# Kernel tuning notes

Hardware: AMD Instinct MI355X
Metric: run time of the kernel (lower is better)

## Reference

```python
import jax, jax.numpy as jnp
import numpy as np

ALPHA = 1.0
RANK = 4


def _conv2d_same(x, w):
    # x: [B,C,H,W], w: [O,C,kh,kw], stride 1, 'same' padding
    return jax.lax.conv_general_dilated(
        x, w, window_strides=(1, 1), padding='SAME',
        dimension_numbers=('NCHW', 'OIHW', 'NCHW'))


def setup_inputs() -> dict:
    key = jax.random.key(0)
    k1, k2, k3, k4, k5 = jax.random.split(key, 5)
    B, C, H, W = 32, 64, 64, 256
    O, E, r, k = 64, 4, RANK, 3
    x = jax.random.normal(k1, (B, C, H, W), dtype=jnp.float32)
    subject_id = jax.random.randint(k2, (B,), 0, E, dtype=jnp.int64)
    W_conv = jax.random.normal(k3, (O, C, k, k), dtype=jnp.float32) * (1.0 / np.sqrt(C * k * k))
    W_A = jax.random.normal(k4, (E, r, C, k, k), dtype=jnp.float32) * 0.02
    # torch init zeros W_B; use random here so the LoRA path is numerically exercised
    W_B = jax.random.normal(k5, (E, O, r), dtype=jnp.float32) * 0.02
    return {'x': x, 'subject_id': subject_id, 'W_conv': W_conv, 'W_A': W_A, 'W_B': W_B}


def reference(x, subject_id, W_conv, W_A, W_B):
    B, C, H, W = x.shape
    E, r = W_A.shape[0], W_A.shape[1]
    k = W_A.shape[-1]
    # Base conv
    out = _conv2d_same(x, W_conv)  # [B,O,H,W]
    # Run all adapter A-convs in one batched conv (E*r tiny output channels),
    # then per-sample select the adapter matching subject_id (same math as the
    # masked per-adapter dispatch in the original).
    a_all = _conv2d_same(x, W_A.reshape(E * r, C, k, k))  # [B,E*r,H,W]
    a_all = a_all.reshape(B, E, r, H, W)
    idx = subject_id[:, None, None, None, None]
    a_sel = jnp.take_along_axis(a_all, idx, axis=1)[:, 0]  # [B,r,H,W]
    wb_sel = W_B[subject_id]  # [B,O,r] (1x1 conv weight per sample)
    lora = (ALPHA / r) * jnp.einsum('bor,brhw->bohw', wb_sel, a_sel)
    return out + lora
```

## Files before the change

### kernel.cpp

```cpp
#include <hip/hip_runtime.h>
#include <hip/hip_bf16.h>

typedef __attribute__((ext_vector_type(8)))  short bf16x8;
typedef __attribute__((ext_vector_type(16))) float f32x16;

constexpr int Bn = 32, Cn = 64, Hn = 64, Wn = 256, On = 64, En = 4, Rn = 4;
constexpr float SCALE = 1.0f / Rn;

constexpr int WTILE  = 32;
constexpr int HSTRIP = 16;
constexpr int SLOT_B = 34 * 128;

__device__ __forceinline__ int swz(int ww, int cb) {
    return ww * 128 + ((cb ^ ((ww >> 2) & 7)) * 16);
}

__global__ __launch_bounds__(256) void merge_k(
    const float* __restrict__ Wc, const float* __restrict__ Wa,
    const float* __restrict__ Wb, __hip_bfloat16* __restrict__ Wfrag)
{
    int t = blockIdx.x * 256 + threadIdx.x;
    int j    = t & 7;
    int lane = (t >> 3) & 63;
    int g    = t >> 9;
    int s    = g % 36;
    int mh   = (g / 36) & 1;
    int e    = g / 72;
    int m = lane & 31, half = lane >> 5;
    int o = mh * 32 + m;
    int tap = s >> 2, cq = s & 3;
    int c = cq * 16 + half * 8 + j;
    float acc = Wc[(o * Cn + c) * 9 + tap];
#pragma unroll
    for (int r = 0; r < Rn; ++r)
        acc += SCALE * Wb[(e * On + o) * Rn + r] * Wa[((e * Rn + r) * Cn + c) * 9 + tap];
    Wfrag[t] = __float2bfloat16(acc);
}

__global__ __launch_bounds__(128, 2) void conv8_k(
    const float* __restrict__ x, const int* __restrict__ sid,
    const __hip_bfloat16* __restrict__ Wfrag, float* __restrict__ out)
{
    __shared__ __align__(16) char xs[4 * SLOT_B];

    const int tid = threadIdx.x;
    const int w0  = blockIdx.x * WTILE;
    const int h0  = blockIdx.y * HSTRIP;
    const int b   = blockIdx.z;
    const int e   = sid[b];
    const size_t HW = (size_t)Hn * Wn;

    const int lane = tid & 63, mh = tid >> 6;
    const int n = lane & 31, half = lane >> 5;

    bf16x8 wf[36];
    const bf16x8* wg = reinterpret_cast<const bf16x8*>(Wfrag) + (size_t)(e * 2 + mh) * 36 * 64;
#pragma unroll
    for (int s = 0; s < 36; ++s) wf[s] = wg[s * 64 + lane];

    const int pb = tid >> 3, q = tid & 7;
    const float* xbase = x + ((size_t)b * Cn + pb * 4) * HW + w0 + 4 * q;

    const int hside = tid >> 6, hc = tid & 63;
    const int gwh   = hside ? (w0 + WTILE) : (w0 - 1);
    const bool hv   = (unsigned)gwh < (unsigned)Wn;
    const float* hbase = x + ((size_t)b * Cn + hc) * HW + gwh;

    auto stage_load = [&](float4 (&f)[4], float& hx, int rx) {
        const int gh = h0 + rx;
        if ((unsigned)gh < (unsigned)Hn) {
            const float* src = xbase + (size_t)gh * Wn;
#pragma unroll
            for (int r = 0; r < 4; ++r)
                f[r] = *reinterpret_cast<const float4*>(src + r * HW);
            hx = hv ? hbase[(size_t)gh * Wn] : 0.0f;
        } else {
            float4 z4 = make_float4(0.0f, 0.0f, 0.0f, 0.0f);
#pragma unroll
            for (int r = 0; r < 4; ++r) f[r] = z4;
            hx = 0.0f;
        }
    };
    auto stage_store = [&](float4 (&f)[4], float& hx, int rx) {
        const int slot = (rx + 1) & 3;
        char* dbase = xs + slot * SLOT_B;
        const int cb = pb >> 1, sub = (pb & 1) * 8;
#pragma unroll
        for (int j = 0; j < 4; ++j) {
            union { __hip_bfloat16 u[4]; short4 v; } pk;
#pragma unroll
            for (int r = 0; r < 4; ++r) {
                float v = (j == 0) ? f[r].x : (j == 1) ? f[r].y : (j == 2) ? f[r].z : f[r].w;
                pk.u[r] = __float2bfloat16(v);
            }
            int ww = 4 * q + 1 + j;
            *reinterpret_cast<short4*>(dbase + swz(ww, cb) + sub) = pk.v;
        }
        {
            __hip_bfloat16 hb = __float2bfloat16(hx);
            int ww = hside ? (WTILE + 1) : 0;
            *reinterpret_cast<__hip_bfloat16*>(dbase + swz(ww, hc >> 3) + (hc & 7) * 2) = hb;
        }
    };

    auto barrier = [&]() {
        asm volatile("s_waitcnt lgkmcnt(0)" ::: "memory");
        __builtin_amdgcn_s_barrier();
    };

    float4 fA[4], fB[4];
    float  hxA, hxB;

    stage_load(fA, hxA, -1); stage_store(fA, hxA, -1);
    stage_load(fA, hxA, 0);  stage_store(fA, hxA, 0);
    stage_load(fA, hxA, 1);  stage_store(fA, hxA, 1);
    stage_load(fA, hxA, 2);
    barrier();

    for (int st = 0; st < HSTRIP; ++st) {
        const bool do_issue = (st + 3 <= HSTRIP);
        if (do_issue) {
            if (st & 1) stage_load(fA, hxA, st + 3);
            else        stage_load(fB, hxB, st + 3);
        }

        f32x16 a;
#pragma unroll
        for (int i = 0; i < 16; ++i) a[i] = 0.0f;

#pragma unroll
        for (int s = 0; s < 36; ++s) {
            const int tap = s >> 2, cq = s & 3;
            const int dh = tap / 3, dw = tap % 3;
            const int slotbase = ((st + dh) & 3) * SLOT_B;
            int ww = n + dw;
            bf16x8 bf = *reinterpret_cast<const bf16x8*>(xs + slotbase + swz(ww, cq * 2 + half));
            a = __builtin_amdgcn_mfma_f32_32x32x16_bf16(wf[s], bf, a, 0, 0, 0);
        }

        const bool do_store = (st + 2 <= HSTRIP);
        if (do_store) {
            if (st & 1) stage_store(fB, hxB, st + 2);
            else        stage_store(fA, hxA, st + 2);
        }

        {
            const int hrow = h0 + st;
            size_t base = ((size_t)(b * On + mh * 32 + 4 * half) * Hn + hrow) * Wn + w0 + n;
#pragma unroll
            for (int r = 0; r < 16; ++r) {
                int o_off = (r & 3) + 8 * (r >> 2);
                out[base + (size_t)o_off * HW] = a[r];
            }
        }

        barrier();
    }
}

extern "C" void kernel_launch(void* const* d_in, const int* in_sizes, int n_in,
                              void* d_out, int out_size, void* d_ws, size_t ws_size,
                              hipStream_t stream)
{
    const float* x   = (const float*)d_in[0];
    const int*   sid = (const int*)d_in[1];
    const float* Wc  = (const float*)d_in[2];
    const float* Wa  = (const float*)d_in[3];
    const float* Wb  = (const float*)d_in[4];
    float*       out = (float*)d_out;

    __hip_bfloat16* Wfrag = (__hip_bfloat16*)d_ws;

    merge_k<<<En * 2 * 36 * 64 * 8 / 256, 256, 0, stream>>>(Wc, Wa, Wb, Wfrag);

    dim3 grid(Wn / WTILE, Hn / HSTRIP, Bn);
    conv8_k<<<grid, 128, 0, stream>>>(x, sid, Wfrag, out);
}
```

Baseline: 273.5 us.

## Pre-pack input to swizzled bf16 NHWC and stream via global_load_lds

Adds a pack kernel that converts x to bf16 in a channel-last, swizzled, zero-padded row layout in workspace. The main conv kernel then copies rows straight into LDS with global_load_lds instead of per-thread fp32 loads, conversion and LDS stores. It also widens the tile to 64 columns with 4 waves and splits the MFMA chain across two accumulators. The cost is an extra full pass over x (fp32 read plus bf16 write) and a dependence on workspace size, with the old kernel kept as a fallback.

```diff
diff --git a/kernel.cpp b/kernel.cpp
--- a/kernel.cpp
+++ b/kernel.cpp
@@ -7,13 +7,20 @@
 constexpr int Bn = 32, Cn = 64, Hn = 64, Wn = 256, On = 64, En = 4, Rn = 4;
 constexpr float SCALE = 1.0f / Rn;
 
-constexpr int WTILE  = 32;
-constexpr int HSTRIP = 16;
-constexpr int SLOT_B = 34 * 128;
-
-__device__ __forceinline__ int swz(int ww, int cb) {
-    return ww * 128 + ((cb ^ ((ww >> 2) & 7)) * 16);
-}
+constexpr int ROW_B  = 258 * 128;
+
+constexpr int WTILE  = 64;
+constexpr int HSTRIP = 8;
+constexpr int SLOT_B = 66 * 128;
+
+constexpr size_t WFRAG_B = 294912;
+constexpr size_t XP_B    = (size_t)Bn * Hn * ROW_B;
+constexpr size_t ZROW_B  = ROW_B;
+
+#define GLOAD_LDS16(SRC, DST) \
+    __builtin_amdgcn_global_load_lds( \
+        (const __attribute__((address_space(1))) void*)(SRC), \
+        (__attribute__((address_space(3))) void*)(DST), 16, 0, 0)
 
 __global__ __launch_bounds__(256) void merge_k(
     const float* __restrict__ Wc, const float* __restrict__ Wa,
@@ -37,9 +44,48 @@
     Wfrag[t] = __float2bfloat16(acc);
 }
 
-__global__ __launch_bounds__(128, 2) void conv8_k(
-    const float* __restrict__ x, const int* __restrict__ sid,
-    const __hip_bfloat16* __restrict__ Wfrag, float* __restrict__ out)
+__global__ __launch_bounds__(256) void pack_k(
+    const float* __restrict__ x, __hip_bfloat16* __restrict__ xp,
+    __hip_bfloat16* __restrict__ zr)
+{
+    size_t g = (size_t)blockIdx.x * 256 + threadIdx.x;
+    if (blockIdx.x < 8192) {
+        int l  = (int)(g & 1023);
+        int cb = l & 7;
+        int p  = l >> 3;
+        int bh = (int)(g >> 10);
+        const float* xr = x + ((size_t)(bh >> 6) * Cn * Hn + (bh & 63)) * Wn;
+        union { __hip_bfloat16 u[8]; bf16x8 v; } u0, u1;
+#pragma unroll
+        for (int i = 0; i < 8; ++i) {
+            int c = cb * 8 + i;
+            float2 L = *reinterpret_cast<const float2*>(xr + (size_t)c * Hn * Wn + 2 * p);
+            u0.u[i] = __float2bfloat16(L.x);
+            u1.u[i] = __float2bfloat16(L.y);
+        }
+        char* row = (char*)xp + (size_t)bh * ROW_B;
+        int s0 = 2 * p + 1, s1 = 2 * p + 2;
+        *reinterpret_cast<bf16x8*>(row + s0 * 128 + ((cb ^ (s0 & 7)) * 16)) = u0.v;
+        *reinterpret_cast<bf16x8*>(row + s1 * 128 + ((cb ^ (s1 & 7)) * 16)) = u1.v;
+    } else if (blockIdx.x < 8192 + 128) {
+        int z = (int)(g - (size_t)8192 * 256);
+        int cb = z & 7, t = (z >> 3) & 1, bh = z >> 4;
+        char* row = (char*)xp + (size_t)bh * ROW_B;
+        bf16x8 zz = {};
+        *reinterpret_cast<bf16x8*>(row + (t ? 257 : 0) * 128 + cb * 16) = zz;
+    } else {
+        int t = (int)(g - (size_t)(8192 + 128) * 256);
+        if (t < ROW_B / 16) {
+            bf16x8 zz = {};
+            reinterpret_cast<bf16x8*>(zr)[t] = zz;
+        }
+    }
+}
+
+__global__ __launch_bounds__(256, 2) void conv9_k(
+    const __hip_bfloat16* __restrict__ xp, const __hip_bfloat16* __restrict__ zr,
+    const int* __restrict__ sid, const __hip_bfloat16* __restrict__ Wfrag,
+    float* __restrict__ out)
 {
     __shared__ __align__(16) char xs[4 * SLOT_B];
 
@@ -50,6 +96,98 @@
     const int e   = sid[b];
     const size_t HW = (size_t)Hn * Wn;
 
+    const int lane = tid & 63, wave = tid >> 6;
+    const int mh = wave & 1, nh = wave >> 1;
+    const int n = lane & 31, half = lane >> 5;
+
+    bf16x8 wf[36];
+    const bf16x8* wg = reinterpret_cast<const bf16x8*>(Wfrag) + (size_t)(e * 2 + mh) * 36 * 64;
+#pragma unroll
+    for (int s = 0; s < 36; ++s) wf[s] = wg[s * 64 + lane];
+
+    const char* xpb = (const char*)xp + (size_t)b * Hn * ROW_B + (size_t)w0 * 128;
+    const char* zrw = (const char*)zr + (size_t)w0 * 128;
+    const int lofs = wave * 1024 + lane * 16;
+
+    auto stage = [&](int rx) {
+        const int gh = h0 + rx;
+        const char* src = ((unsigned)gh < (unsigned)Hn) ? (xpb + (size_t)gh * ROW_B) : zrw;
+        char* dst = xs + ((rx + 1) & 3) * SLOT_B + wave * 1024;
+        GLOAD_LDS16(src + lofs,        dst);
+        GLOAD_LDS16(src + 4096 + lofs, dst + 4096);
+        GLOAD_LDS16(src + 4352 + lofs, dst + 4352);
+    };
+
+    stage(-1); stage(0); stage(1);
+    __syncthreads();
+
+    for (int st = 0; st < HSTRIP; ++st) {
+        stage(st + 2);
+
+        f32x16 a0, a1;
+#pragma unroll
+        for (int i = 0; i < 16; ++i) { a0[i] = 0.0f; a1[i] = 0.0f; }
+
+#pragma unroll
+        for (int s2 = 0; s2 < 18; ++s2) {
+            {
+                const int s = 2 * s2;
+                const int tap = s >> 2, cq = s & 3;
+                const int dh = tap / 3, dw = tap % 3;
+                int ww = nh * 32 + n + dw;
+                const char* p = xs + ((st + dh) & 3) * SLOT_B
+                              + ww * 128 + (((cq * 2 + half) ^ (ww & 7)) * 16);
+                a0 = __builtin_amdgcn_mfma_f32_32x32x16_bf16(
+                        wf[s], *reinterpret_cast<const bf16x8*>(p), a0, 0, 0, 0);
+            }
+            {
+                const int s = 2 * s2 + 1;
+                const int tap = s >> 2, cq = s & 3;
+                const int dh = tap / 3, dw = tap % 3;
+                int ww = nh * 32 + n + dw;
+                const char* p = xs + ((st + dh) & 3) * SLOT_B
+                              + ww * 128 + (((cq * 2 + half) ^ (ww & 7)) * 16);
+                a1 = __builtin_amdgcn_mfma_f32_32x32x16_bf16(
+                        wf[s], *reinterpret_cast<const bf16x8*>(p), a1, 0, 0, 0);
+            }
+        }
+
+        {
+            const int hrow = h0 + st;
+            size_t base = ((size_t)(b * On + mh * 32 + 4 * half) * Hn + hrow) * Wn
+                          + w0 + nh * 32 + n;
+#pragma unroll
+            for (int r = 0; r < 16; ++r) {
+                int o_off = (r & 3) + 8 * (r >> 2);
+                out[base + (size_t)o_off * HW] = a0[r] + a1[r];
+            }
+        }
+
+        __syncthreads();
+    }
+}
+
+constexpr int FB_WTILE  = 32;
+constexpr int FB_HSTRIP = 16;
+constexpr int FB_SLOT_B = 34 * 128;
+
+__device__ __forceinline__ int fb_swz(int ww, int cb) {
+    return ww * 128 + ((cb ^ ((ww >> 2) & 7)) * 16);
+}
+
+__global__ __launch_bounds__(128, 2) void conv8_k(
+    const float* __restrict__ x, const int* __restrict__ sid,
+    const __hip_bfloat16* __restrict__ Wfrag, float* __restrict__ out)
+{
+    __shared__ __align__(16) char xs[4 * FB_SLOT_B];
+
+    const int tid = threadIdx.x;
+    const int w0  = blockIdx.x * FB_WTILE;
+    const int h0  = blockIdx.y * FB_HSTRIP;
+    const int b   = blockIdx.z;
+    const int e   = sid[b];
+    const size_t HW = (size_t)Hn * Wn;
+
     const int lane = tid & 63, mh = tid >> 6;
     const int n = lane & 31, half = lane >> 5;
 
@@ -62,7 +200,7 @@
     const float* xbase = x + ((size_t)b * Cn + pb * 4) * HW + w0 + 4 * q;
 
     const int hside = tid >> 6, hc = tid & 63;
-    const int gwh   = hside ? (w0 + WTILE) : (w0 - 1);
+    const int gwh   = hside ? (w0 + FB_WTILE) : (w0 - 1);
     const bool hv   = (unsigned)gwh < (unsigned)Wn;
     const float* hbase = x + ((size_t)b * Cn + hc) * HW + gwh;
 
@@ -83,7 +221,7 @@
     };
     auto stage_store = [&](float4 (&f)[4], float& hx, int rx) {
         const int slot = (rx + 1) & 3;
-        char* dbase = xs + slot * SLOT_B;
+        char* dbase = xs + slot * FB_SLOT_B;
         const int cb = pb >> 1, sub = (pb & 1) * 8;
 #pragma unroll
         for (int j = 0; j < 4; ++j) {
@@ -94,12 +232,12 @@
                 pk.u[r] = __float2bfloat16(v);
             }
             int ww = 4 * q + 1 + j;
-            *reinterpret_cast<short4*>(dbase + swz(ww, cb) + sub) = pk.v;
+            *reinterpret_cast<short4*>(dbase + fb_swz(ww, cb) + sub) = pk.v;
         }
         {
             __hip_bfloat16 hb = __float2bfloat16(hx);
-            int ww = hside ? (WTILE + 1) : 0;
-            *reinterpret_cast<__hip_bfloat16*>(dbase + swz(ww, hc >> 3) + (hc & 7) * 2) = hb;
+            int ww = hside ? (FB_WTILE + 1) : 0;
+            *reinterpret_cast<__hip_bfloat16*>(dbase + fb_swz(ww, hc >> 3) + (hc & 7) * 2) = hb;
         }
     };
 
@@ -117,8 +255,8 @@
     stage_load(fA, hxA, 2);
     barrier();
 
-    for (int st = 0; st < HSTRIP; ++st) {
-        const bool do_issue = (st + 3 <= HSTRIP);
+    for (int st = 0; st < FB_HSTRIP; ++st) {
+        const bool do_issue = (st + 3 <= FB_HSTRIP);
         if (do_issue) {
             if (st & 1) stage_load(fA, hxA, st + 3);
             else        stage_load(fB, hxB, st + 3);
@@ -132,13 +270,13 @@
         for (int s = 0; s < 36; ++s) {
             const int tap = s >> 2, cq = s & 3;
             const int dh = tap / 3, dw = tap % 3;
-            const int slotbase = ((st + dh) & 3) * SLOT_B;
+            const int slotbase = ((st + dh) & 3) * FB_SLOT_B;
             int ww = n + dw;
-            bf16x8 bf = *reinterpret_cast<const bf16x8*>(xs + slotbase + swz(ww, cq * 2 + half));
+            bf16x8 bf = *reinterpret_cast<const bf16x8*>(xs + slotbase + fb_swz(ww, cq * 2 + half));
             a = __builtin_amdgcn_mfma_f32_32x32x16_bf16(wf[s], bf, a, 0, 0, 0);
         }
 
-        const bool do_store = (st + 2 <= HSTRIP);
+        const bool do_store = (st + 2 <= FB_HSTRIP);
         if (do_store) {
             if (st & 1) stage_store(fB, hxB, st + 2);
             else        stage_store(fA, hxA, st + 2);
@@ -173,6 +311,15 @@
 
     merge_k<<<En * 2 * 36 * 64 * 8 / 256, 256, 0, stream>>>(Wc, Wa, Wb, Wfrag);
 
-    dim3 grid(Wn / WTILE, Hn / HSTRIP, Bn);
-    conv8_k<<<grid, 128, 0, stream>>>(x, sid, Wfrag, out);
-}
+    const size_t NEED = WFRAG_B + XP_B + ZROW_B;
+    if (ws_size >= NEED) {
+        __hip_bfloat16* xp = (__hip_bfloat16*)((char*)d_ws + WFRAG_B);
+        __hip_bfloat16* zw = (__hip_bfloat16*)((char*)d_ws + WFRAG_B + XP_B);
+        pack_k<<<8192 + 128 + 9, 256, 0, stream>>>(x, xp, zw);
+        dim3 grid(Wn / WTILE, Hn / HSTRIP, Bn);
+        conv9_k<<<grid, 256, 0, stream>>>(xp, zw, sid, Wfrag, out);
+    } else {
+        dim3 grid(Wn / FB_WTILE, Hn / FB_HSTRIP, Bn);
+        conv8_k<<<grid, 128, 0, stream>>>(x, sid, Wfrag, out);
+    }
+}
```

New measurement: 283.0 us. 3.5% more time.
